# Kernel tuning notes

Hardware: AMD Instinct MI355X
Metric: run time of the kernel (lower is better)

Reference implementation:

```python
import jax, jax.numpy as jnp
import numpy as np

NUM_USERS = 100000
NUM_ITEMS = 50000
EMB = 64
N_SOC = 1000000
N_RAT = 1000000
BATCH = 16384
EPS = 1e-8


def setup_inputs() -> dict:
    key = jax.random.key(0)
    ks = jax.random.split(key, 8)
    user_emb = 0.01 * jax.random.normal(ks[0], (NUM_USERS, EMB), jnp.float32)
    item_emb = 0.01 * jax.random.normal(ks[1], (NUM_ITEMS, EMB), jnp.float32)
    users = jax.random.randint(ks[2], (BATCH,), 0, NUM_USERS)
    items = jax.random.randint(ks[3], (BATCH,), 0, NUM_ITEMS)
    social_src = jax.random.randint(ks[4], (N_SOC,), 0, NUM_USERS)
    social_dst = jax.random.randint(ks[5], (N_SOC,), 0, NUM_USERS)
    like_u = jax.random.randint(ks[6], (N_RAT,), 0, NUM_USERS)
    like_i = jax.random.randint(ks[7], (N_RAT,), 0, NUM_ITEMS)
    return {"user_emb": user_emb, "item_emb": item_emb, "users": users,
            "items": items, "social_src": social_src, "social_dst": social_dst,
            "like_u": like_u, "like_i": like_i}


def _deg(idx, num):
    # node degree as float column vector [num, 1]
    return jax.ops.segment_sum(jnp.ones((idx.shape[0],), jnp.float32), idx,
                               num_segments=num)[:, None]


def _seg_mean(msg, idx, num):
    s = jax.ops.segment_sum(msg, idx, num_segments=num)
    cnt = _deg(idx, num)
    return s / jnp.maximum(cnt, 1.0)


def reference(user_emb, item_emb, users, items, social_src, social_dst, like_u, like_i):
    # degree-based self-weights (deg=0 -> 1, deg>0 -> ~0)
    user_deg = _deg(like_u, NUM_USERS)            # out-degree on 'like'
    u_sw = 1.0 - user_deg / (user_deg + EPS)
    item_deg = _deg(like_i, NUM_ITEMS)            # out-degree on 'rev_like'
    i_sw = 1.0 - item_deg / (item_deg + EPS)

    def social_conv(hu):
        # mean aggregation over user->user social edges
        return _seg_mean(hu[social_src], social_dst, NUM_USERS)

    def rating_conv(hu, hi):
        # user <- mean of liked-item embeddings, plus degree-gated self
        new_u = u_sw * hu + _seg_mean(hi[like_i], like_u, NUM_USERS)
        new_i = i_sw * hi + _seg_mean(hu[like_u], like_i, NUM_ITEMS)
        return new_u, new_i

    # layer 1
    soc1 = social_conv(user_emb)
    rat_u1, rat_i1 = rating_conv(user_emb, item_emb)
    u1 = 0.5 * soc1 + 0.5 * rat_u1
    # layer 2 (stacked on per-branch states, as in the torch code)
    soc2 = social_conv(soc1)
    rat_u2, _ = rating_conv(rat_u1, rat_i1)
    u2 = 0.5 * soc2 + 0.5 * rat_u2

    # l_user = [0, 1, 2]
    final_user = user_emb + u1 + u2
    final_item = item_emb

    latest_user = final_user[users]
    latest_item = final_item[items]
    predict = jax.nn.sigmoid(jnp.sum(latest_user * latest_item, axis=1))
    return predict, latest_user, latest_item
```

## Files before the change

### kernel.cpp

```cpp
#include <hip/hip_runtime.h>
#include <hip/hip_bf16.h>

#define NUSERS 100000
#define NITEMS 50000
#define NEDGE  1000000
#define NBATCH 16384
#define CAP_LU 320000
#define EPB    2048
#define NBLK_E ((NEDGE + EPB - 1) / EPB)
#define NBW    3125
#define GGRID  2048
#define NB_CVT 9375
#define NB_INIT (NB_CVT + (NBATCH + 255) / 256)

#define OFF_GC     0
#define OFF_GB     768
#define OFF_GCUR   1536
#define OFF_BITS   2304
#define OFF_NEED   (OFF_BITS + 3136)
#define OFF_ZEND   (OFF_NEED + NUSERS / 4)
#define OFF_IDEG   OFF_ZEND
#define OFF_UDEG   (OFF_IDEG + NITEMS)
#define OFF_SDEG   (OFF_UDEG + NUSERS)
#define OFF_ISTART (OFF_SDEG + NUSERS)
#define OFF_USTART (OFF_ISTART + NITEMS)
#define OFF_SSTART (OFF_USTART + NUSERS)
#define OFF_UEMBH  530464
#define OFF_REC    (OFF_UEMBH + NUSERS * 32)
#define OFF_SOC1   (OFF_REC + NITEMS * 64)
#define OFF_PARTLI (OFF_SOC1 + NUSERS * 32)
#define OFF_PARTLU (OFF_PARTLI + NEDGE)
#define OFF_PARTSD (OFF_PARTLU + CAP_LU)
#define OFF_CSRLI  (OFF_PARTSD + NEDGE)
#define OFF_CSRLU  (OFF_CSRLI + NEDGE)
#define OFF_CSRSD  (OFF_CSRLU + CAP_LU)
#define WS_FLOATS  (OFF_CSRSD + NEDGE)

typedef unsigned short u16;

__device__ __forceinline__ float bf2f(u16 h) {
    union { unsigned u; float f; } c; c.u = ((unsigned)h) << 16; return c.f;
}
__device__ __forceinline__ u16 f2bf(float f) {
    union { float f; unsigned u; } c; c.f = f;
    unsigned r = c.u + 0x7fffu + ((c.u >> 16) & 1u);
    return (u16)(r >> 16);
}
__device__ __forceinline__ void acc2(unsigned w, float& a0, float& a1) {
    a0 += bf2f((u16)(w & 0xffff));
    a1 += bf2f((u16)(w >> 16));
}
__device__ __forceinline__ void acc8(uint4 w, float* a) {
    acc2(w.x, a[0], a[1]); acc2(w.y, a[2], a[3]);
    acc2(w.z, a[4], a[5]); acc2(w.w, a[6], a[7]);
}

__global__ void k_init(const float* __restrict__ uemb, const float* __restrict__ iemb,
                       const int* __restrict__ users, u16* __restrict__ uembh,
                       u16* __restrict__ rec, unsigned* __restrict__ bits,
                       unsigned char* __restrict__ needed) {
    int blk = blockIdx.x;
    if (blk < NB_CVT) {
        int t = blk * 256 + threadIdx.x;
        if (t < NUSERS * 16) {
            float4 v = ((const float4*)uemb)[t];
            ushort4 o;
            o.x = f2bf(v.x); o.y = f2bf(v.y); o.z = f2bf(v.z); o.w = f2bf(v.w);
            ((ushort4*)uembh)[t] = o;
        } else {
            int t2 = t - NUSERS * 16;
            int i = t2 >> 4, c = t2 & 15;
            float4 v = ((const float4*)iemb)[t2];
            ushort4 o;
            o.x = f2bf(v.x); o.y = f2bf(v.y); o.z = f2bf(v.z); o.w = f2bf(v.w);
            ((ushort4*)rec)[i * 32 + c] = o;
        }
    } else {
        int b = (blk - NB_CVT) * 256 + threadIdx.x;
        if (b < NBATCH) {
            int u = users[b];
            atomicOr(&bits[u >> 5], 1u << (u & 31));
            needed[u] = 1;
        }
    }
}

__global__ void k_passA(const int* __restrict__ lu, const int* __restrict__ li,
                        const int* __restrict__ sd, const int* __restrict__ ss,
                        const unsigned* __restrict__ bits, int* __restrict__ gcnt,
                        unsigned char* __restrict__ needed) {
    __shared__ int lc[768];
    __shared__ unsigned sbits[NBW];
    int t = threadIdx.x;
    for (int k = t; k < 768; k += 256) lc[k] = 0;
    for (int k = t; k < NBW; k += 256) sbits[k] = bits[k];
    __syncthreads();
    int base = blockIdx.x * EPB;
    int end = base + EPB; if (end > NEDGE) end = NEDGE;
    for (int e = base + t; e < end; e += 256) {
        int item = li[e], a = lu[e], d = sd[e];
        atomicAdd(&lc[item >> 9], 1);
        if ((sbits[a >> 5] >> (a & 31)) & 1)
            atomicAdd(&lc[256 + (a >> 9)], 1);
        atomicAdd(&lc[512 + (d >> 9)], 1);
        if ((sbits[d >> 5] >> (d & 31)) & 1)
            needed[ss[e]] = 1;
    }
    __syncthreads();
    for (int k = t; k < 768; k += 256)
        if (lc[k]) atomicAdd(&gcnt[k], lc[k]);
}

__global__ void k_passB(const int* __restrict__ gcnt, int* __restrict__ gbase,
                        int* __restrict__ gcur) {
    __shared__ int s[256];
    int t = threadIdx.x;
    for (int j = 0; j < 3; ++j) {
        int v = gcnt[j * 256 + t];
        s[t] = v;
        __syncthreads();
        for (int o = 1; o < 256; o <<= 1) {
            int x = (t >= o) ? s[t - o] : 0;
            __syncthreads();
            s[t] += x;
            __syncthreads();
        }
        int ex = s[t] - v;
        gbase[j * 256 + t] = ex;
        gcur[j * 256 + t] = ex;
        __syncthreads();
    }
}

__global__ void k_passC(const int* __restrict__ lu, const int* __restrict__ li,
                        const int* __restrict__ sd, const int* __restrict__ ss,
                        const unsigned* __restrict__ bits, int* __restrict__ gcur,
                        int* __restrict__ partLI, int* __restrict__ partLU,
                        int* __restrict__ partSD) {
    __shared__ int lc[768];
    __shared__ int go[768];
    __shared__ unsigned sbits[NBW];
    int t = threadIdx.x;
    for (int k = t; k < 768; k += 256) lc[k] = 0;
    for (int k = t; k < NBW; k += 256) sbits[k] = bits[k];
    __syncthreads();
    int base = blockIdx.x * EPB;
    int end = base + EPB; if (end > NEDGE) end = NEDGE;
    unsigned mask = 0;
    int i = 0;
    for (int e = base + t; e < end; e += 256, ++i) {
        int item = li[e], a = lu[e], d = sd[e];
        atomicAdd(&lc[item >> 9], 1);
        if ((sbits[a >> 5] >> (a & 31)) & 1) {
            atomicAdd(&lc[256 + (a >> 9)], 1);
            mask |= (1u << i);
        }
        atomicAdd(&lc[512 + (d >> 9)], 1);
    }
    __syncthreads();
    for (int k = t; k < 768; k += 256) {
        go[k] = lc[k] ? atomicAdd(&gcur[k], lc[k]) : 0;
        lc[k] = 0;
    }
    __syncthreads();
    i = 0;
    for (int e = base + t; e < end; e += 256, ++i) {
        int item = li[e], a = lu[e], d = sd[e], s_ = ss[e];
        int b0 = item >> 9;
        int r0 = atomicAdd(&lc[b0], 1);
        partLI[go[b0] + r0] = (a << 9) | (item & 511);
        if (mask & (1u << i)) {
            int b1 = 256 + (a >> 9);
            int r1 = atomicAdd(&lc[b1], 1);
            partLU[go[b1] + r1] = (item << 9) | (a & 511);
        }
        int b2 = 512 + (d >> 9);
        int r2 = atomicAdd(&lc[b2], 1);
        partSD[go[b2] + r2] = (s_ << 9) | (d & 511);
    }
}

__global__ void k_passD(const int* __restrict__ gcnt, const int* __restrict__ gbase,
                        const int* __restrict__ partLI, const int* __restrict__ partLU,
                        const int* __restrict__ partSD, int* __restrict__ csrli,
                        int* __restrict__ csrlu, int* __restrict__ csrsd,
                        int* __restrict__ ideg, int* __restrict__ udeg,
                        int* __restrict__ sdeg, int* __restrict__ istart,
                        int* __restrict__ ustart, int* __restrict__ sstart) {
    __shared__ int lcnt[512], lstart[512], sb[2][512];
    int t = threadIdx.x;
    int blk = blockIdx.x, list, b;
    const int* part; int* csr; int* deg; int* start; int n;
    if (blk < 196)      { list = 0; b = blk;       part = partLI; csr = csrli; deg = ideg; start = istart; n = NITEMS; }
    else if (blk < 392) { list = 1; b = blk - 196; part = partLU; csr = csrlu; deg = udeg; start = ustart; n = NUSERS; }
    else                { list = 2; b = blk - 392; part = partSD; csr = csrsd; deg = sdeg; start = sstart; n = NUSERS; }
    int base = gbase[list * 256 + b], cnt = gcnt[list * 256 + b];
    int node0 = b << 9;
    int M = n - node0; if (M > 512) M = 512; if (M < 0) M = 0;

    lcnt[t] = 0; lcnt[t + 256] = 0;
    __syncthreads();
    for (int i = t; i < cnt; i += 256) atomicAdd(&lcnt[part[base + i] & 511], 1);
    __syncthreads();
    sb[0][t] = lcnt[t]; sb[0][t + 256] = lcnt[t + 256];
    __syncthreads();
    int pp = 0;
    for (int o = 1; o < 512; o <<= 1) {
        int np = pp ^ 1;
        for (int k = t; k < 512; k += 256) {
            int v = sb[pp][k];
            if (k >= o) v += sb[pp][k - o];
            sb[np][k] = v;
        }
        __syncthreads();
        pp = np;
    }
    for (int k = t; k < 512; k += 256) {
        int ex = sb[pp][k] - lcnt[k];
        lstart[k] = ex;
        if (k < M) { deg[node0 + k] = lcnt[k]; start[node0 + k] = base + ex; }
    }
    __syncthreads();
    lcnt[t] = 0; lcnt[t + 256] = 0;
    __syncthreads();
    for (int i = t; i < cnt; i += 256) {
        int p = part[base + i];
        int nl = p & 511;
        int r = atomicAdd(&lcnt[nl], 1);
        csr[base + lstart[nl] + r] = p >> 9;
    }
}

__device__ __forceinline__ void item_store(int n, int dg, const float* __restrict__ iemb,
                                           u16* __restrict__ rec, int l8,
                                           const float* __restrict__ s) {
    float dgf = (float)dg;
    float inv = 1.0f / fmaxf(dgf, 1.0f);
    float sw  = 1.0f - dgf / (dgf + 1e-8f);
    float4 e0 = ((const float4*)(iemb + n * 64))[l8 * 2];
    float4 e1 = ((const float4*)(iemb + n * 64))[l8 * 2 + 1];
    uint4 o;
    o.x = (unsigned)f2bf(sw * e0.x + s[0] * inv) | ((unsigned)f2bf(sw * e0.y + s[1] * inv) << 16);
    o.y = (unsigned)f2bf(sw * e0.z + s[2] * inv) | ((unsigned)f2bf(sw * e0.w + s[3] * inv) << 16);
    o.z = (unsigned)f2bf(sw * e1.x + s[4] * inv) | ((unsigned)f2bf(sw * e1.y + s[5] * inv) << 16);
    o.w = (unsigned)f2bf(sw * e1.z + s[6] * inv) | ((unsigned)f2bf(sw * e1.w + s[7] * inv) << 16);
    ((uint4*)(rec + n * 128 + 64))[l8] = o;
}
__device__ __forceinline__ void soc_store(int n, int dg, unsigned* __restrict__ soc1, int l8,
                                          const float* __restrict__ s) {
    float inv = 1.0f / fmaxf((float)dg, 1.0f);
    uint4 o;
    o.x = (unsigned)f2bf(s[0] * inv) | ((unsigned)f2bf(s[1] * inv) << 16);
    o.y = (unsigned)f2bf(s[2] * inv) | ((unsigned)f2bf(s[3] * inv) << 16);
    o.z = (unsigned)f2bf(s[4] * inv) | ((unsigned)f2bf(s[5] * inv) << 16);
    o.w = (unsigned)f2bf(s[6] * inv) | ((unsigned)f2bf(s[7] * inv) << 16);
    ((uint4*)(soc1 + n * 32))[l8] = o;
}

__device__ __forceinline__ void gather_pair(const unsigned* __restrict__ uh32,
                                            const int* __restrict__ csr,
                                            int jA, int dA, int jB, int dB,
                                            int lane, int g, int l8,
                                            float* __restrict__ aA,
                                            float* __restrict__ aB) {
    int cA = (lane < dA) ? csr[jA + lane] : 0;
    int cB = (lane < dB) ? csr[jB + lane] : 0;
    int kmA = dA < 64 ? dA : 64;
    int kmB = dB < 64 ? dB : 64;
    int clA = kmA > 0 ? kmA - 1 : 0;
    int clB = kmB > 0 ? kmB - 1 : 0;
    int km  = kmA > kmB ? kmA : kmB;
    for (int k = 0; k < km; k += 16) {
        int q0 = k + g, q1 = k + 8 + g;
        int iA0 = q0 < kmA ? q0 : clA;
        int iA1 = q1 < kmA ? q1 : clA;
        int iB0 = q0 < kmB ? q0 : clB;
        int iB1 = q1 < kmB ? q1 : clB;
        int rA0 = __shfl(cA, iA0), rA1 = __shfl(cA, iA1);
        int rB0 = __shfl(cB, iB0), rB1 = __shfl(cB, iB1);
        uint4 wA0 = *(const uint4*)(uh32 + rA0 * 32 + l8 * 4);
        uint4 wA1 = *(const uint4*)(uh32 + rA1 * 32 + l8 * 4);
        uint4 wB0 = *(const uint4*)(uh32 + rB0 * 32 + l8 * 4);
        uint4 wB1 = *(const uint4*)(uh32 + rB1 * 32 + l8 * 4);
        if (q0 < kmA) acc8(wA0, aA);
        if (q1 < kmA) acc8(wA1, aA);
        if (q0 < kmB) acc8(wB0, aB);
        if (q1 < kmB) acc8(wB1, aB);
    }
    for (int k = 64; k < dA; k += 8) {
        int q = k + g; int idx = q < dA ? q : dA - 1;
        int r = csr[jA + idx];
        uint4 w = *(const uint4*)(uh32 + r * 32 + l8 * 4);
        if (q < dA) acc8(w, aA);
    }
    for (int k = 64; k < dB; k += 8) {
        int q = k + g; int idx = q < dB ? q : dB - 1;
        int r = csr[jB + idx];
        uint4 w = *(const uint4*)(uh32 + r * 32 + l8 * 4);
        if (q < dB) acc8(w, aB);
    }
    #pragma unroll
    for (int off = 8; off <= 32; off <<= 1) {
        #pragma unroll
        for (int m = 0; m < 8; ++m) {
            aA[m] += __shfl_xor(aA[m], off);
            aB[m] += __shfl_xor(aB[m], off);
        }
    }
}

__global__ void k_gather_fused(const float* __restrict__ iemb,
                               const unsigned* __restrict__ uh32,
                               const int* __restrict__ csrli, const int* __restrict__ istart,
                               const int* __restrict__ ideg, u16* __restrict__ rec,
                               const int* __restrict__ csrsd, const int* __restrict__ sstart,
                               const int* __restrict__ sdeg,
                               const unsigned char* __restrict__ needed,
                               unsigned* __restrict__ soc1) {
    int lane = threadIdx.x & 63;
    int wid  = blockIdx.x * 4 + (threadIdx.x >> 6);
    int nw   = gridDim.x * 4;
    int g = lane >> 3, l8 = lane & 7;
    const int NPI = NITEMS / 2;
    const int NP  = NPI + NUSERS / 2;
    for (int w = wid; w < NP; w += nw) {
        if (w < NPI) {
            int nA = w * 2, nB = nA + 1;
            int jA = istart[nA], dA = ideg[nA];
            int jB = istart[nB], dB = ideg[nB];
            float aA[8] = {0.f,0.f,0.f,0.f,0.f,0.f,0.f,0.f};
            float aB[8] = {0.f,0.f,0.f,0.f,0.f,0.f,0.f,0.f};
            gather_pair(uh32, csrli, jA, dA, jB, dB, lane, g, l8, aA, aB);
            if (g == 0)      item_store(nA, dA, iemb, rec, l8, aA);
            else if (g == 1) item_store(nB, dB, iemb, rec, l8, aB);
        } else {
            int nA = (w - NPI) * 2, nB = nA + 1;
            unsigned short nd = *(const unsigned short*)(needed + nA);
            if (!nd) continue;
            int needA = nd & 0xff, needB = nd >> 8;
            int jA = sstart[nA], dA = needA ? sdeg[nA] : 0;
            int jB = sstart[nB], dB = needB ? sdeg[nB] : 0;
            float aA[8] = {0.f,0.f,0.f,0.f,0.f,0.f,0.f,0.f};
            float aB[8] = {0.f,0.f,0.f,0.f,0.f,0.f,0.f,0.f};
            gather_pair(uh32, csrsd, jA, dA, jB, dB, lane, g, l8, aA, aB);
            if (g == 0 && needA)      soc_store(nA, dA, soc1, l8, aA);
            else if (g == 1 && needB) soc_store(nB, dB, soc1, l8, aB);
        }
    }
}

__global__ void k_final2(const int* __restrict__ users, const int* __restrict__ items,
                         const float* __restrict__ uemb, const float* __restrict__ iemb,
                         const u16* __restrict__ rec, const int* __restrict__ csrlu,
                         const int* __restrict__ ustart, const int* __restrict__ udeg,
                         const u16* __restrict__ soc1, const int* __restrict__ csrsd,
                         const int* __restrict__ sstart, const int* __restrict__ sdeg,
                         float* __restrict__ out) {
    int d   = threadIdx.x & 63;
    int wid = blockIdx.x * 4 + (threadIdx.x >> 6);
    if (wid >= NBATCH / 2) return;
    int bA = wid, bB = wid + NBATCH / 2;
    int uA = users[bA], uB = users[bB];
    int itA = items[bA], itB = items[bB];
    int juA = ustart[uA], duA = udeg[uA];
    int juB = ustart[uB], duB = udeg[uB];
    int jsA = sstart[uA], dsA = sdeg[uA];
    int jsB = sstart[uB], dsB = sdeg[uB];
    int cvUA = (d < duA) ? csrlu[juA + d] : 0;
    int cvUB = (d < duB) ? csrlu[juB + d] : 0;
    int cvSA = (d < dsA) ? csrsd[jsA + d] : 0;
    int cvSB = (d < dsB) ? csrsd[jsB + d] : 0;
    int kmuA = duA < 64 ? duA : 64, cluA = kmuA > 0 ? kmuA - 1 : 0;
    int kmuB = duB < 64 ? duB : 64, cluB = kmuB > 0 ? kmuB - 1 : 0;
    int kmu = kmuA > kmuB ? kmuA : kmuB;
    float pA0=0.f,pA1=0.f,pA2=0.f,pA3=0.f, qA0=0.f,qA1=0.f,qA2=0.f,qA3=0.f;
    float pB0=0.f,pB1=0.f,pB2=0.f,pB3=0.f, qB0=0.f,qB1=0.f,qB2=0.f,qB3=0.f;
    for (int k = 0; k < kmu; k += 4) {
        int xA0 = k   < kmuA ? k   : cluA, xA1 = k+1 < kmuA ? k+1 : cluA;
        int xA2 = k+2 < kmuA ? k+2 : cluA, xA3 = k+3 < kmuA ? k+3 : cluA;
        int xB0 = k   < kmuB ? k   : cluB, xB1 = k+1 < kmuB ? k+1 : cluB;
        int xB2 = k+2 < kmuB ? k+2 : cluB, xB3 = k+3 < kmuB ? k+3 : cluB;
        int iA0 = __shfl(cvUA, xA0), iA1 = __shfl(cvUA, xA1);
        int iA2 = __shfl(cvUA, xA2), iA3 = __shfl(cvUA, xA3);
        int iB0 = __shfl(cvUB, xB0), iB1 = __shfl(cvUB, xB1);
        int iB2 = __shfl(cvUB, xB2), iB3 = __shfl(cvUB, xB3);
        float tA0 = bf2f(rec[iA0*128 + d]),    tA1 = bf2f(rec[iA1*128 + d]);
        float tA2 = bf2f(rec[iA2*128 + d]),    tA3 = bf2f(rec[iA3*128 + d]);
        float rA0 = bf2f(rec[iA0*128 + 64 + d]), rA1 = bf2f(rec[iA1*128 + 64 + d]);
        float rA2 = bf2f(rec[iA2*128 + 64 + d]), rA3 = bf2f(rec[iA3*128 + 64 + d]);
        float tB0 = bf2f(rec[iB0*128 + d]),    tB1 = bf2f(rec[iB1*128 + d]);
        float tB2 = bf2f(rec[iB2*128 + d]),    tB3 = bf2f(rec[iB3*128 + d]);
        float rB0 = bf2f(rec[iB0*128 + 64 + d]), rB1 = bf2f(rec[iB1*128 + 64 + d]);
        float rB2 = bf2f(rec[iB2*128 + 64 + d]), rB3 = bf2f(rec[iB3*128 + 64 + d]);
        if (k   < kmuA) { pA0 += tA0; qA0 += rA0; }
        if (k+1 < kmuA) { pA1 += tA1; qA1 += rA1; }
        if (k+2 < kmuA) { pA2 += tA2; qA2 += rA2; }
        if (k+3 < kmuA) { pA3 += tA3; qA3 += rA3; }
        if (k   < kmuB) { pB0 += tB0; qB0 += rB0; }
        if (k+1 < kmuB) { pB1 += tB1; qB1 += rB1; }
        if (k+2 < kmuB) { pB2 += tB2; qB2 += rB2; }
        if (k+3 < kmuB) { pB3 += tB3; qB3 += rB3; }
    }
    for (int j = juA + 64; j < juA + duA; ++j) {
        int i0 = csrlu[j];
        pA0 += bf2f(rec[i0*128 + d]); qA0 += bf2f(rec[i0*128 + 64 + d]);
    }
    for (int j = juB + 64; j < juB + duB; ++j) {
        int i0 = csrlu[j];
        pB0 += bf2f(rec[i0*128 + d]); qB0 += bf2f(rec[i0*128 + 64 + d]);
    }
    int kmsA = dsA < 64 ? dsA : 64, clsA = kmsA > 0 ? kmsA - 1 : 0;
    int kmsB = dsB < 64 ? dsB : 64, clsB = kmsB > 0 ? kmsB - 1 : 0;
    int kms = kmsA > kmsB ? kmsA : kmsB;
    float sA0=0.f,sA1=0.f,sA2=0.f,sA3=0.f, sB0=0.f,sB1=0.f,sB2=0.f,sB3=0.f;
    for (int k = 0; k < kms; k += 4) {
        int xA0 = k   < kmsA ? k   : clsA, xA1 = k+1 < kmsA ? k+1 : clsA;
        int xA2 = k+2 < kmsA ? k+2 : clsA, xA3 = k+3 < kmsA ? k+3 : clsA;
        int xB0 = k   < kmsB ? k   : clsB, xB1 = k+1 < kmsB ? k+1 : clsB;
        int xB2 = k+2 < kmsB ? k+2 : clsB, xB3 = k+3 < kmsB ? k+3 : clsB;
        int cA0 = __shfl(cvSA, xA0), cA1 = __shfl(cvSA, xA1);
        int cA2 = __shfl(cvSA, xA2), cA3 = __shfl(cvSA, xA3);
        int cB0 = __shfl(cvSB, xB0), cB1 = __shfl(cvSB, xB1);
        int cB2 = __shfl(cvSB, xB2), cB3 = __shfl(cvSB, xB3);
        float fA0 = bf2f(soc1[cA0*64 + d]), fA1 = bf2f(soc1[cA1*64 + d]);
        float fA2 = bf2f(soc1[cA2*64 + d]), fA3 = bf2f(soc1[cA3*64 + d]);
        float fB0 = bf2f(soc1[cB0*64 + d]), fB1 = bf2f(soc1[cB1*64 + d]);
        float fB2 = bf2f(soc1[cB2*64 + d]), fB3 = bf2f(soc1[cB3*64 + d]);
        if (k   < kmsA) sA0 += fA0;
        if (k+1 < kmsA) sA1 += fA1;
        if (k+2 < kmsA) sA2 += fA2;
        if (k+3 < kmsA) sA3 += fA3;
        if (k   < kmsB) sB0 += fB0;
        if (k+1 < kmsB) sB1 += fB1;
        if (k+2 < kmsB) sB2 += fB2;
        if (k+3 < kmsB) sB3 += fB3;
    }
    for (int j = jsA + 64; j < jsA + dsA; ++j)
        sA0 += bf2f(soc1[csrsd[j]*64 + d]);
    for (int j = jsB + 64; j < jsB + dsB; ++j)
        sB0 += bf2f(soc1[csrsd[j]*64 + d]);
    {
        float invU = 1.0f / fmaxf((float)duA, 1.0f);
        float ru1 = ((pA0 + pA1) + (pA2 + pA3)) * invU;
        float ru2 = ((qA0 + qA1) + (qA2 + qA3)) * invU;
        float s2 = ((sA0 + sA1) + (sA2 + sA3)) / fmaxf((float)dsA, 1.0f);
        float ud = (float)duA;
        float usw = 1.0f - ud / (ud + 1e-8f);
        float ue = uemb[uA * 64 + d];
        float s1 = bf2f(soc1[uA * 64 + d]);
        float r1 = usw * ue + ru1;
        float r2 = usw * r1 + ru2;
        float fu = ue + 0.5f * (s1 + r1) + 0.5f * (s2 + r2);
        float iv = iemb[itA * 64 + d];
        out[NBATCH + bA * 64 + d]               = fu;
        out[NBATCH + NBATCH * 64 + bA * 64 + d] = iv;
        float p = fu * iv;
        #pragma unroll
        for (int o = 32; o > 0; o >>= 1) p += __shfl_down(p, o);
        if (d == 0) out[bA] = 1.0f / (1.0f + __expf(-p));
    }
    {
        float invU = 1.0f / fmaxf((float)duB, 1.0f);
        float ru1 = ((pB0 + pB1) + (pB2 + pB3)) * invU;
        float ru2 = ((qB0 + qB1) + (qB2 + qB3)) * invU;
        float s2 = ((sB0 + sB1) + (sB2 + sB3)) / fmaxf((float)dsB, 1.0f);
        float ud = (float)duB;
        float usw = 1.0f - ud / (ud + 1e-8f);
        float ue = uemb[uB * 64 + d];
        float s1 = bf2f(soc1[uB * 64 + d]);
        float r1 = usw * ue + ru1;
        float r2 = usw * r1 + ru2;
        float fu = ue + 0.5f * (s1 + r1) + 0.5f * (s2 + r2);
        float iv = iemb[itB * 64 + d];
        out[NBATCH + bB * 64 + d]               = fu;
        out[NBATCH + NBATCH * 64 + bB * 64 + d] = iv;
        float p = fu * iv;
        #pragma unroll
        for (int o = 32; o > 0; o >>= 1) p += __shfl_down(p, o);
        if (d == 0) out[bB] = 1.0f / (1.0f + __expf(-p));
    }
}

extern "C" void kernel_launch(void* const* d_in, const int* in_sizes, int n_in,
                              void* d_out, int out_size, void* d_ws, size_t ws_size,
                              hipStream_t stream) {
    const float* uemb  = (const float*)d_in[0];
    const float* iemb  = (const float*)d_in[1];
    const int*   users = (const int*)d_in[2];
    const int*   items = (const int*)d_in[3];
    const int*   ssrc  = (const int*)d_in[4];
    const int*   sdst  = (const int*)d_in[5];
    const int*   lu    = (const int*)d_in[6];
    const int*   li    = (const int*)d_in[7];
    float* out = (float*)d_out;

    if (ws_size < (size_t)WS_FLOATS * 4) return;

    int*           W      = (int*)d_ws;
    int*           gcnt   = W + OFF_GC;
    int*           gbase  = W + OFF_GB;
    int*           gcur   = W + OFF_GCUR;
    unsigned*      bits   = (unsigned*)(W + OFF_BITS);
    unsigned char* needed = (unsigned char*)(W + OFF_NEED);
    int*           ideg   = W + OFF_IDEG;
    int*           udeg   = W + OFF_UDEG;
    int*           sdeg   = W + OFF_SDEG;
    int*           istart = W + OFF_ISTART;
    int*           ustart = W + OFF_USTART;
    int*           sstart = W + OFF_SSTART;
    u16*           uembh  = (u16*)(W + OFF_UEMBH);
    u16*           rec    = (u16*)(W + OFF_REC);
    u16*           soc1   = (u16*)(W + OFF_SOC1);
    int*           partLI = W + OFF_PARTLI;
    int*           partLU = W + OFF_PARTLU;
    int*           partSD = W + OFF_PARTSD;
    int*           csrli  = W + OFF_CSRLI;
    int*           csrlu  = W + OFF_CSRLU;
    int*           csrsd  = W + OFF_CSRSD;

    hipMemsetAsync(d_ws, 0, (size_t)OFF_ZEND * 4, stream);

    const int B = 256;

    k_init<<<NB_INIT, B, 0, stream>>>(uemb, iemb, users, uembh, rec, bits, needed);

    k_passA<<<NBLK_E, B, 0, stream>>>(lu, li, sdst, ssrc, bits, gcnt, needed);
    k_passB<<<1, B, 0, stream>>>(gcnt, gbase, gcur);
    k_passC<<<NBLK_E, B, 0, stream>>>(lu, li, sdst, ssrc, bits, gcur,
                                      partLI, partLU, partSD);
    k_passD<<<588, B, 0, stream>>>(gcnt, gbase, partLI, partLU, partSD,
                                   csrli, csrlu, csrsd, ideg, udeg, sdeg,
                                   istart, ustart, sstart);

    k_gather_fused<<<GGRID, B, 0, stream>>>(iemb, (const unsigned*)uembh,
                                            csrli, istart, ideg, rec,
                                            csrsd, sstart, sdeg, needed,
                                            (unsigned*)soc1);

    k_final2<<<2048, B, 0, stream>>>(users, items, uemb, iemb, rec, csrlu,
                                     ustart, udeg, soc1, csrsd, sstart, sdeg, out);
}
```

Baseline: 254.2 us.

## Fuse all graph phases into one cooperative persistent kernel with grid syncs

Turns the memset plus seven separate kernel launches into a single cooperative kernel. The phases (zero/convert, slot marking, bucket count, scan, scatter, CSR build, gather, final) run as grid-stride loops separated by grid.sync(). The intent is to remove per-launch overhead and inter-kernel gaps. In exchange, parallelism is capped at the cooperative grid size (at most 1024 blocks), and the grid-wide barriers have their own cost. A non-cooperative multi-kernel fallback path is kept.

```diff
diff --git a/kernel.cpp b/kernel.cpp
--- a/kernel.cpp
+++ b/kernel.cpp
@@ -1,5 +1,8 @@
 #include <hip/hip_runtime.h>
 #include <hip/hip_bf16.h>
+#include <hip/hip_cooperative_groups.h>
+
+namespace cg = cooperative_groups;
 
 #define NUSERS 100000
 #define NITEMS 50000
@@ -10,8 +13,7 @@
 #define NBLK_E ((NEDGE + EPB - 1) / EPB)
 #define NBW    3125
 #define GGRID  2048
-#define NB_CVT 9375
-#define NB_INIT (NB_CVT + (NBATCH + 255) / 256)
+#define CGRID  1024
 
 #define OFF_GC     0
 #define OFF_GB     768
@@ -36,6 +38,8 @@
 #define OFF_CSRSD  (OFF_CSRLU + CAP_LU)
 #define WS_FLOATS  (OFF_CSRSD + NEDGE)
 
+#define SMEM_INTS  4661
+
 typedef unsigned short u16;
 
 __device__ __forceinline__ float bf2f(u16 h) {
@@ -55,13 +59,15 @@
     acc2(w.z, a[4], a[5]); acc2(w.w, a[6], a[7]);
 }
 
-__global__ void k_init(const float* __restrict__ uemb, const float* __restrict__ iemb,
-                       const int* __restrict__ users, u16* __restrict__ uembh,
-                       u16* __restrict__ rec, unsigned* __restrict__ bits,
-                       unsigned char* __restrict__ needed) {
-    int blk = blockIdx.x;
-    if (blk < NB_CVT) {
-        int t = blk * 256 + threadIdx.x;
+
+__device__ void ph_zero_cvt(const float* __restrict__ uemb, const float* __restrict__ iemb,
+                            int* __restrict__ W, u16* __restrict__ uembh,
+                            u16* __restrict__ rec) {
+    int tid = blockIdx.x * blockDim.x + threadIdx.x;
+    int nthr = gridDim.x * blockDim.x;
+    for (int k = tid; k < OFF_ZEND; k += nthr) W[k] = 0;
+    const int NT = (NUSERS + NITEMS) * 16;
+    for (int t = tid; t < NT; t += nthr) {
         if (t < NUSERS * 16) {
             float4 v = ((const float4*)uemb)[t];
             ushort4 o;
@@ -75,45 +81,53 @@
             o.x = f2bf(v.x); o.y = f2bf(v.y); o.z = f2bf(v.z); o.w = f2bf(v.w);
             ((ushort4*)rec)[i * 32 + c] = o;
         }
-    } else {
-        int b = (blk - NB_CVT) * 256 + threadIdx.x;
-        if (b < NBATCH) {
-            int u = users[b];
-            atomicOr(&bits[u >> 5], 1u << (u & 31));
-            needed[u] = 1;
-        }
-    }
-}
-
-__global__ void k_passA(const int* __restrict__ lu, const int* __restrict__ li,
-                        const int* __restrict__ sd, const int* __restrict__ ss,
-                        const unsigned* __restrict__ bits, int* __restrict__ gcnt,
+    }
+}
+
+__device__ void ph_slot(const int* __restrict__ users, unsigned* __restrict__ bits,
                         unsigned char* __restrict__ needed) {
-    __shared__ int lc[768];
-    __shared__ unsigned sbits[NBW];
+    int tid = blockIdx.x * blockDim.x + threadIdx.x;
+    int nthr = gridDim.x * blockDim.x;
+    for (int b = tid; b < NBATCH; b += nthr) {
+        int u = users[b];
+        atomicOr(&bits[u >> 5], 1u << (u & 31));
+        needed[u] = 1;
+    }
+}
+
+__device__ void ph_passA(int* __restrict__ smem, const int* __restrict__ lu,
+                         const int* __restrict__ li, const int* __restrict__ sd,
+                         const int* __restrict__ ss, const unsigned* __restrict__ bits,
+                         int* __restrict__ gcnt, unsigned char* __restrict__ needed) {
     int t = threadIdx.x;
-    for (int k = t; k < 768; k += 256) lc[k] = 0;
+    int* lc = smem;
+    unsigned* sbits = (unsigned*)(smem + 768);
     for (int k = t; k < NBW; k += 256) sbits[k] = bits[k];
-    __syncthreads();
-    int base = blockIdx.x * EPB;
-    int end = base + EPB; if (end > NEDGE) end = NEDGE;
-    for (int e = base + t; e < end; e += 256) {
-        int item = li[e], a = lu[e], d = sd[e];
-        atomicAdd(&lc[item >> 9], 1);
-        if ((sbits[a >> 5] >> (a & 31)) & 1)
-            atomicAdd(&lc[256 + (a >> 9)], 1);
-        atomicAdd(&lc[512 + (d >> 9)], 1);
-        if ((sbits[d >> 5] >> (d & 31)) & 1)
-            needed[ss[e]] = 1;
-    }
-    __syncthreads();
-    for (int k = t; k < 768; k += 256)
-        if (lc[k]) atomicAdd(&gcnt[k], lc[k]);
-}
-
-__global__ void k_passB(const int* __restrict__ gcnt, int* __restrict__ gbase,
-                        int* __restrict__ gcur) {
-    __shared__ int s[256];
+    for (int vb = blockIdx.x; vb < NBLK_E; vb += gridDim.x) {
+        for (int k = t; k < 768; k += 256) lc[k] = 0;
+        __syncthreads();
+        int base = vb * EPB;
+        int end = base + EPB; if (end > NEDGE) end = NEDGE;
+        for (int e = base + t; e < end; e += 256) {
+            int item = li[e], a = lu[e], d = sd[e];
+            atomicAdd(&lc[item >> 9], 1);
+            if ((sbits[a >> 5] >> (a & 31)) & 1)
+                atomicAdd(&lc[256 + (a >> 9)], 1);
+            atomicAdd(&lc[512 + (d >> 9)], 1);
+            if ((sbits[d >> 5] >> (d & 31)) & 1)
+                needed[ss[e]] = 1;
+        }
+        __syncthreads();
+        for (int k = t; k < 768; k += 256)
+            if (lc[k]) atomicAdd(&gcnt[k], lc[k]);
+        __syncthreads();
+    }
+}
+
+__device__ void ph_passB(const int* __restrict__ gcnt, int* __restrict__ gbase,
+                         int* __restrict__ gcur, int* __restrict__ smem) {
+    if (blockIdx.x != 0) return;
+    int* s = smem;
     int t = threadIdx.x;
     for (int j = 0; j < 3; ++j) {
         int v = gcnt[j * 256 + t];
@@ -132,102 +146,110 @@
     }
 }
 
-__global__ void k_passC(const int* __restrict__ lu, const int* __restrict__ li,
-                        const int* __restrict__ sd, const int* __restrict__ ss,
-                        const unsigned* __restrict__ bits, int* __restrict__ gcur,
-                        int* __restrict__ partLI, int* __restrict__ partLU,
-                        int* __restrict__ partSD) {
-    __shared__ int lc[768];
-    __shared__ int go[768];
-    __shared__ unsigned sbits[NBW];
+__device__ void ph_passC(int* __restrict__ smem, const int* __restrict__ lu,
+                         const int* __restrict__ li, const int* __restrict__ sd,
+                         const int* __restrict__ ss, const unsigned* __restrict__ bits,
+                         int* __restrict__ gcur, int* __restrict__ partLI,
+                         int* __restrict__ partLU, int* __restrict__ partSD) {
     int t = threadIdx.x;
-    for (int k = t; k < 768; k += 256) lc[k] = 0;
+    int* lc = smem;
+    int* go = smem + 768;
+    unsigned* sbits = (unsigned*)(smem + 1536);
     for (int k = t; k < NBW; k += 256) sbits[k] = bits[k];
-    __syncthreads();
-    int base = blockIdx.x * EPB;
-    int end = base + EPB; if (end > NEDGE) end = NEDGE;
-    unsigned mask = 0;
-    int i = 0;
-    for (int e = base + t; e < end; e += 256, ++i) {
-        int item = li[e], a = lu[e], d = sd[e];
-        atomicAdd(&lc[item >> 9], 1);
-        if ((sbits[a >> 5] >> (a & 31)) & 1) {
-            atomicAdd(&lc[256 + (a >> 9)], 1);
-            mask |= (1u << i);
-        }
-        atomicAdd(&lc[512 + (d >> 9)], 1);
-    }
-    __syncthreads();
-    for (int k = t; k < 768; k += 256) {
-        go[k] = lc[k] ? atomicAdd(&gcur[k], lc[k]) : 0;
-        lc[k] = 0;
-    }
-    __syncthreads();
-    i = 0;
-    for (int e = base + t; e < end; e += 256, ++i) {
-        int item = li[e], a = lu[e], d = sd[e], s_ = ss[e];
-        int b0 = item >> 9;
-        int r0 = atomicAdd(&lc[b0], 1);
-        partLI[go[b0] + r0] = (a << 9) | (item & 511);
-        if (mask & (1u << i)) {
-            int b1 = 256 + (a >> 9);
-            int r1 = atomicAdd(&lc[b1], 1);
-            partLU[go[b1] + r1] = (item << 9) | (a & 511);
-        }
-        int b2 = 512 + (d >> 9);
-        int r2 = atomicAdd(&lc[b2], 1);
-        partSD[go[b2] + r2] = (s_ << 9) | (d & 511);
-    }
-}
-
-__global__ void k_passD(const int* __restrict__ gcnt, const int* __restrict__ gbase,
-                        const int* __restrict__ partLI, const int* __restrict__ partLU,
-                        const int* __restrict__ partSD, int* __restrict__ csrli,
-                        int* __restrict__ csrlu, int* __restrict__ csrsd,
-                        int* __restrict__ ideg, int* __restrict__ udeg,
-                        int* __restrict__ sdeg, int* __restrict__ istart,
-                        int* __restrict__ ustart, int* __restrict__ sstart) {
-    __shared__ int lcnt[512], lstart[512], sb[2][512];
+    for (int vb = blockIdx.x; vb < NBLK_E; vb += gridDim.x) {
+        for (int k = t; k < 768; k += 256) lc[k] = 0;
+        __syncthreads();
+        int base = vb * EPB;
+        int end = base + EPB; if (end > NEDGE) end = NEDGE;
+        unsigned mask = 0;
+        int i = 0;
+        for (int e = base + t; e < end; e += 256, ++i) {
+            int item = li[e], a = lu[e], d = sd[e];
+            atomicAdd(&lc[item >> 9], 1);
+            if ((sbits[a >> 5] >> (a & 31)) & 1) {
+                atomicAdd(&lc[256 + (a >> 9)], 1);
+                mask |= (1u << i);
+            }
+            atomicAdd(&lc[512 + (d >> 9)], 1);
+        }
+        __syncthreads();
+        for (int k = t; k < 768; k += 256) {
+            go[k] = lc[k] ? atomicAdd(&gcur[k], lc[k]) : 0;
+            lc[k] = 0;
+        }
+        __syncthreads();
+        i = 0;
+        for (int e = base + t; e < end; e += 256, ++i) {
+            int item = li[e], a = lu[e], d = sd[e], s_ = ss[e];
+            int b0 = item >> 9;
+            int r0 = atomicAdd(&lc[b0], 1);
+            partLI[go[b0] + r0] = (a << 9) | (item & 511);
+            if (mask & (1u << i)) {
+                int b1 = 256 + (a >> 9);
+                int r1 = atomicAdd(&lc[b1], 1);
+                partLU[go[b1] + r1] = (item << 9) | (a & 511);
+            }
+            int b2 = 512 + (d >> 9);
+            int r2 = atomicAdd(&lc[b2], 1);
+            partSD[go[b2] + r2] = (s_ << 9) | (d & 511);
+        }
+        __syncthreads();
+    }
+}
+
+__device__ void ph_passD(int* __restrict__ smem, const int* __restrict__ gcnt,
+                         const int* __restrict__ gbase, const int* __restrict__ partLI,
+                         const int* __restrict__ partLU, const int* __restrict__ partSD,
+                         int* __restrict__ csrli, int* __restrict__ csrlu,
+                         int* __restrict__ csrsd, int* __restrict__ ideg,
+                         int* __restrict__ udeg, int* __restrict__ sdeg,
+                         int* __restrict__ istart, int* __restrict__ ustart,
+                         int* __restrict__ sstart) {
     int t = threadIdx.x;
-    int blk = blockIdx.x, list, b;
-    const int* part; int* csr; int* deg; int* start; int n;
-    if (blk < 196)      { list = 0; b = blk;       part = partLI; csr = csrli; deg = ideg; start = istart; n = NITEMS; }
-    else if (blk < 392) { list = 1; b = blk - 196; part = partLU; csr = csrlu; deg = udeg; start = ustart; n = NUSERS; }
-    else                { list = 2; b = blk - 392; part = partSD; csr = csrsd; deg = sdeg; start = sstart; n = NUSERS; }
-    int base = gbase[list * 256 + b], cnt = gcnt[list * 256 + b];
-    int node0 = b << 9;
-    int M = n - node0; if (M > 512) M = 512; if (M < 0) M = 0;
-
-    lcnt[t] = 0; lcnt[t + 256] = 0;
-    __syncthreads();
-    for (int i = t; i < cnt; i += 256) atomicAdd(&lcnt[part[base + i] & 511], 1);
-    __syncthreads();
-    sb[0][t] = lcnt[t]; sb[0][t + 256] = lcnt[t + 256];
-    __syncthreads();
-    int pp = 0;
-    for (int o = 1; o < 512; o <<= 1) {
-        int np = pp ^ 1;
+    int* lcnt = smem;
+    int* lstart = smem + 512;
+    for (int blk = blockIdx.x; blk < 588; blk += gridDim.x) {
+        int list, b;
+        const int* part; int* csr; int* deg; int* start; int n;
+        if (blk < 196)      { list = 0; b = blk;       part = partLI; csr = csrli; deg = ideg; start = istart; n = NITEMS; }
+        else if (blk < 392) { list = 1; b = blk - 196; part = partLU; csr = csrlu; deg = udeg; start = ustart; n = NUSERS; }
+        else                { list = 2; b = blk - 392; part = partSD; csr = csrsd; deg = sdeg; start = sstart; n = NUSERS; }
+        int base = gbase[list * 256 + b], cnt = gcnt[list * 256 + b];
+        int node0 = b << 9;
+        int M = n - node0; if (M > 512) M = 512; if (M < 0) M = 0;
+
+        lcnt[t] = 0; lcnt[t + 256] = 0;
+        __syncthreads();
+        for (int i = t; i < cnt; i += 256) atomicAdd(&lcnt[part[base + i] & 511], 1);
+        __syncthreads();
+        int* ps = smem + 1024;
+        int* pd = smem + 1536;
+        ps[t] = lcnt[t]; ps[t + 256] = lcnt[t + 256];
+        __syncthreads();
+        for (int o = 1; o < 512; o <<= 1) {
+            for (int k = t; k < 512; k += 256) {
+                int v = ps[k];
+                if (k >= o) v += ps[k - o];
+                pd[k] = v;
+            }
+            __syncthreads();
+            int* tmp = ps; ps = pd; pd = tmp;
+        }
         for (int k = t; k < 512; k += 256) {
-            int v = sb[pp][k];
-            if (k >= o) v += sb[pp][k - o];
-            sb[np][k] = v;
-        }
-        __syncthreads();
-        pp = np;
-    }
-    for (int k = t; k < 512; k += 256) {
-        int ex = sb[pp][k] - lcnt[k];
-        lstart[k] = ex;
-        if (k < M) { deg[node0 + k] = lcnt[k]; start[node0 + k] = base + ex; }
-    }
-    __syncthreads();
-    lcnt[t] = 0; lcnt[t + 256] = 0;
-    __syncthreads();
-    for (int i = t; i < cnt; i += 256) {
-        int p = part[base + i];
-        int nl = p & 511;
-        int r = atomicAdd(&lcnt[nl], 1);
-        csr[base + lstart[nl] + r] = p >> 9;
+            int ex = ps[k] - lcnt[k];
+            lstart[k] = ex;
+            if (k < M) { deg[node0 + k] = lcnt[k]; start[node0 + k] = base + ex; }
+        }
+        __syncthreads();
+        lcnt[t] = 0; lcnt[t + 256] = 0;
+        __syncthreads();
+        for (int i = t; i < cnt; i += 256) {
+            int p = part[base + i];
+            int nl = p & 511;
+            int r = atomicAdd(&lcnt[nl], 1);
+            csr[base + lstart[nl] + r] = p >> 9;
+        }
+        __syncthreads();
     }
 }
 
@@ -309,14 +331,13 @@
     }
 }
 
-__global__ void k_gather_fused(const float* __restrict__ iemb,
-                               const unsigned* __restrict__ uh32,
-                               const int* __restrict__ csrli, const int* __restrict__ istart,
-                               const int* __restrict__ ideg, u16* __restrict__ rec,
-                               const int* __restrict__ csrsd, const int* __restrict__ sstart,
-                               const int* __restrict__ sdeg,
-                               const unsigned char* __restrict__ needed,
-                               unsigned* __restrict__ soc1) {
+__device__ void ph_gather(const float* __restrict__ iemb, const unsigned* __restrict__ uh32,
+                          const int* __restrict__ csrli, const int* __restrict__ istart,
+                          const int* __restrict__ ideg, u16* __restrict__ rec,
+                          const int* __restrict__ csrsd, const int* __restrict__ sstart,
+                          const int* __restrict__ sdeg,
+                          const unsigned char* __restrict__ needed,
+                          unsigned* __restrict__ soc1) {
     int lane = threadIdx.x & 63;
     int wid  = blockIdx.x * 4 + (threadIdx.x >> 6);
     int nw   = gridDim.x * 4;
@@ -349,154 +370,147 @@
     }
 }
 
-__global__ void k_final2(const int* __restrict__ users, const int* __restrict__ items,
+__device__ void ph_final(const int* __restrict__ users, const int* __restrict__ items,
                          const float* __restrict__ uemb, const float* __restrict__ iemb,
                          const u16* __restrict__ rec, const int* __restrict__ csrlu,
                          const int* __restrict__ ustart, const int* __restrict__ udeg,
                          const u16* __restrict__ soc1, const int* __restrict__ csrsd,
                          const int* __restrict__ sstart, const int* __restrict__ sdeg,
                          float* __restrict__ out) {
-    int d   = threadIdx.x & 63;
-    int wid = blockIdx.x * 4 + (threadIdx.x >> 6);
-    if (wid >= NBATCH / 2) return;
-    int bA = wid, bB = wid + NBATCH / 2;
-    int uA = users[bA], uB = users[bB];
-    int itA = items[bA], itB = items[bB];
-    int juA = ustart[uA], duA = udeg[uA];
-    int juB = ustart[uB], duB = udeg[uB];
-    int jsA = sstart[uA], dsA = sdeg[uA];
-    int jsB = sstart[uB], dsB = sdeg[uB];
-    int cvUA = (d < duA) ? csrlu[juA + d] : 0;
-    int cvUB = (d < duB) ? csrlu[juB + d] : 0;
-    int cvSA = (d < dsA) ? csrsd[jsA + d] : 0;
-    int cvSB = (d < dsB) ? csrsd[jsB + d] : 0;
-    int kmuA = duA < 64 ? duA : 64, cluA = kmuA > 0 ? kmuA - 1 : 0;
-    int kmuB = duB < 64 ? duB : 64, cluB = kmuB > 0 ? kmuB - 1 : 0;
-    int kmu = kmuA > kmuB ? kmuA : kmuB;
-    float pA0=0.f,pA1=0.f,pA2=0.f,pA3=0.f, qA0=0.f,qA1=0.f,qA2=0.f,qA3=0.f;
-    float pB0=0.f,pB1=0.f,pB2=0.f,pB3=0.f, qB0=0.f,qB1=0.f,qB2=0.f,qB3=0.f;
-    for (int k = 0; k < kmu; k += 4) {
-        int xA0 = k   < kmuA ? k   : cluA, xA1 = k+1 < kmuA ? k+1 : cluA;
-        int xA2 = k+2 < kmuA ? k+2 : cluA, xA3 = k+3 < kmuA ? k+3 : cluA;
-        int xB0 = k   < kmuB ? k   : cluB, xB1 = k+1 < kmuB ? k+1 : cluB;
-        int xB2 = k+2 < kmuB ? k+2 : cluB, xB3 = k+3 < kmuB ? k+3 : cluB;
-        int iA0 = __shfl(cvUA, xA0), iA1 = __shfl(cvUA, xA1);
-        int iA2 = __shfl(cvUA, xA2), iA3 = __shfl(cvUA, xA3);
-        int iB0 = __shfl(cvUB, xB0), iB1 = __shfl(cvUB, xB1);
-        int iB2 = __shfl(cvUB, xB2), iB3 = __shfl(cvUB, xB3);
-        float tA0 = bf2f(rec[iA0*128 + d]),    tA1 = bf2f(rec[iA1*128 + d]);
-        float tA2 = bf2f(rec[iA2*128 + d]),    tA3 = bf2f(rec[iA3*128 + d]);
-        float rA0 = bf2f(rec[iA0*128 + 64 + d]), rA1 = bf2f(rec[iA1*128 + 64 + d]);
-        float rA2 = bf2f(rec[iA2*128 + 64 + d]), rA3 = bf2f(rec[iA3*128 + 64 + d]);
-        float tB0 = bf2f(rec[iB0*128 + d]),    tB1 = bf2f(rec[iB1*128 + d]);
-        float tB2 = bf2f(rec[iB2*128 + d]),    tB3 = bf2f(rec[iB3*128 + d]);
-        float rB0 = bf2f(rec[iB0*128 + 64 + d]), rB1 = bf2f(rec[iB1*128 + 64 + d]);
-        float rB2 = bf2f(rec[iB2*128 + 64 + d]), rB3 = bf2f(rec[iB3*128 + 64 + d]);
-        if (k   < kmuA) { pA0 += tA0; qA0 += rA0; }
-        if (k+1 < kmuA) { pA1 += tA1; qA1 += rA1; }
-        if (k+2 < kmuA) { pA2 += tA2; qA2 += rA2; }
-        if (k+3 < kmuA) { pA3 += tA3; qA3 += rA3; }
-        if (k   < kmuB) { pB0 += tB0; qB0 += rB0; }
-        if (k+1 < kmuB) { pB1 += tB1; qB1 += rB1; }
-        if (k+2 < kmuB) { pB2 += tB2; qB2 += rB2; }
-        if (k+3 < kmuB) { pB3 += tB3; qB3 += rB3; }
-    }
-    for (int j = juA + 64; j < juA + duA; ++j) {
-        int i0 = csrlu[j];
-        pA0 += bf2f(rec[i0*128 + d]); qA0 += bf2f(rec[i0*128 + 64 + d]);
-    }
-    for (int j = juB + 64; j < juB + duB; ++j) {
-        int i0 = csrlu[j];
-        pB0 += bf2f(rec[i0*128 + d]); qB0 += bf2f(rec[i0*128 + 64 + d]);
-    }
-    int kmsA = dsA < 64 ? dsA : 64, clsA = kmsA > 0 ? kmsA - 1 : 0;
-    int kmsB = dsB < 64 ? dsB : 64, clsB = kmsB > 0 ? kmsB - 1 : 0;
-    int kms = kmsA > kmsB ? kmsA : kmsB;
-    float sA0=0.f,sA1=0.f,sA2=0.f,sA3=0.f, sB0=0.f,sB1=0.f,sB2=0.f,sB3=0.f;
-    for (int k = 0; k < kms; k += 4) {
-        int xA0 = k   < kmsA ? k   : clsA, xA1 = k+1 < kmsA ? k+1 : clsA;
-        int xA2 = k+2 < kmsA ? k+2 : clsA, xA3 = k+3 < kmsA ? k+3 : clsA;
-        int xB0 = k   < kmsB ? k   : clsB, xB1 = k+1 < kmsB ? k+1 : clsB;
-        int xB2 = k+2 < kmsB ? k+2 : clsB, xB3 = k+3 < kmsB ? k+3 : clsB;
-        int cA0 = __shfl(cvSA, xA0), cA1 = __shfl(cvSA, xA1);
-        int cA2 = __shfl(cvSA, xA2), cA3 = __shfl(cvSA, xA3);
-        int cB0 = __shfl(cvSB, xB0), cB1 = __shfl(cvSB, xB1);
-        int cB2 = __shfl(cvSB, xB2), cB3 = __shfl(cvSB, xB3);
-        float fA0 = bf2f(soc1[cA0*64 + d]), fA1 = bf2f(soc1[cA1*64 + d]);
-        float fA2 = bf2f(soc1[cA2*64 + d]), fA3 = bf2f(soc1[cA3*64 + d]);
-        float fB0 = bf2f(soc1[cB0*64 + d]), fB1 = bf2f(soc1[cB1*64 + d]);
-        float fB2 = bf2f(soc1[cB2*64 + d]), fB3 = bf2f(soc1[cB3*64 + d]);
-        if (k   < kmsA) sA0 += fA0;
-        if (k+1 < kmsA) sA1 += fA1;
-        if (k+2 < kmsA) sA2 += fA2;
-        if (k+3 < kmsA) sA3 += fA3;
-        if (k   < kmsB) sB0 += fB0;
-        if (k+1 < kmsB) sB1 += fB1;
-        if (k+2 < kmsB) sB2 += fB2;
-        if (k+3 < kmsB) sB3 += fB3;
-    }
-    for (int j = jsA + 64; j < jsA + dsA; ++j)
-        sA0 += bf2f(soc1[csrsd[j]*64 + d]);
-    for (int j = jsB + 64; j < jsB + dsB; ++j)
-        sB0 += bf2f(soc1[csrsd[j]*64 + d]);
-    {
-        float invU = 1.0f / fmaxf((float)duA, 1.0f);
-        float ru1 = ((pA0 + pA1) + (pA2 + pA3)) * invU;
-        float ru2 = ((qA0 + qA1) + (qA2 + qA3)) * invU;
-        float s2 = ((sA0 + sA1) + (sA2 + sA3)) / fmaxf((float)dsA, 1.0f);
-        float ud = (float)duA;
-        float usw = 1.0f - ud / (ud + 1e-8f);
-        float ue = uemb[uA * 64 + d];
-        float s1 = bf2f(soc1[uA * 64 + d]);
-        float r1 = usw * ue + ru1;
-        float r2 = usw * r1 + ru2;
-        float fu = ue + 0.5f * (s1 + r1) + 0.5f * (s2 + r2);
-        float iv = iemb[itA * 64 + d];
-        out[NBATCH + bA * 64 + d]               = fu;
-        out[NBATCH + NBATCH * 64 + bA * 64 + d] = iv;
-        float p = fu * iv;
-        #pragma unroll
-        for (int o = 32; o > 0; o >>= 1) p += __shfl_down(p, o);
-        if (d == 0) out[bA] = 1.0f / (1.0f + __expf(-p));
-    }
-    {
-        float invU = 1.0f / fmaxf((float)duB, 1.0f);
-        float ru1 = ((pB0 + pB1) + (pB2 + pB3)) * invU;
-        float ru2 = ((qB0 + qB1) + (qB2 + qB3)) * invU;
-        float s2 = ((sB0 + sB1) + (sB2 + sB3)) / fmaxf((float)dsB, 1.0f);
-        float ud = (float)duB;
-        float usw = 1.0f - ud / (ud + 1e-8f);
-        float ue = uemb[uB * 64 + d];
-        float s1 = bf2f(soc1[uB * 64 + d]);
-        float r1 = usw * ue + ru1;
-        float r2 = usw * r1 + ru2;
-        float fu = ue + 0.5f * (s1 + r1) + 0.5f * (s2 + r2);
-        float iv = iemb[itB * 64 + d];
-        out[NBATCH + bB * 64 + d]               = fu;
-        out[NBATCH + NBATCH * 64 + bB * 64 + d] = iv;
-        float p = fu * iv;
-        #pragma unroll
-        for (int o = 32; o > 0; o >>= 1) p += __shfl_down(p, o);
-        if (d == 0) out[bB] = 1.0f / (1.0f + __expf(-p));
-    }
-}
-
-extern "C" void kernel_launch(void* const* d_in, const int* in_sizes, int n_in,
-                              void* d_out, int out_size, void* d_ws, size_t ws_size,
-                              hipStream_t stream) {
-    const float* uemb  = (const float*)d_in[0];
-    const float* iemb  = (const float*)d_in[1];
-    const int*   users = (const int*)d_in[2];
-    const int*   items = (const int*)d_in[3];
-    const int*   ssrc  = (const int*)d_in[4];
-    const int*   sdst  = (const int*)d_in[5];
-    const int*   lu    = (const int*)d_in[6];
-    const int*   li    = (const int*)d_in[7];
-    float* out = (float*)d_out;
-
-    if (ws_size < (size_t)WS_FLOATS * 4) return;
-
-    int*           W      = (int*)d_ws;
+    int d    = threadIdx.x & 63;
+    int wid0 = blockIdx.x * 4 + (threadIdx.x >> 6);
+    int nw   = gridDim.x * 4;
+    for (int wid = wid0; wid < NBATCH / 2; wid += nw) {
+        int bA = wid, bB = wid + NBATCH / 2;
+        int uA = users[bA], uB = users[bB];
+        int itA = items[bA], itB = items[bB];
+        int juA = ustart[uA], duA = udeg[uA];
+        int juB = ustart[uB], duB = udeg[uB];
+        int jsA = sstart[uA], dsA = sdeg[uA];
+        int jsB = sstart[uB], dsB = sdeg[uB];
+        int cvUA = (d < duA) ? csrlu[juA + d] : 0;
+        int cvUB = (d < duB) ? csrlu[juB + d] : 0;
+        int cvSA = (d < dsA) ? csrsd[jsA + d] : 0;
+        int cvSB = (d < dsB) ? csrsd[jsB + d] : 0;
+        int kmuA = duA < 64 ? duA : 64, cluA = kmuA > 0 ? kmuA - 1 : 0;
+        int kmuB = duB < 64 ? duB : 64, cluB = kmuB > 0 ? kmuB - 1 : 0;
+        int kmu = kmuA > kmuB ? kmuA : kmuB;
+        float pA0=0.f,pA1=0.f,pA2=0.f,pA3=0.f, qA0=0.f,qA1=0.f,qA2=0.f,qA3=0.f;
+        float pB0=0.f,pB1=0.f,pB2=0.f,pB3=0.f, qB0=0.f,qB1=0.f,qB2=0.f,qB3=0.f;
+        for (int k = 0; k < kmu; k += 4) {
+            int xA0 = k   < kmuA ? k   : cluA, xA1 = k+1 < kmuA ? k+1 : cluA;
+            int xA2 = k+2 < kmuA ? k+2 : cluA, xA3 = k+3 < kmuA ? k+3 : cluA;
+            int xB0 = k   < kmuB ? k   : cluB, xB1 = k+1 < kmuB ? k+1 : cluB;
+            int xB2 = k+2 < kmuB ? k+2 : cluB, xB3 = k+3 < kmuB ? k+3 : cluB;
+            int iA0 = __shfl(cvUA, xA0), iA1 = __shfl(cvUA, xA1);
+            int iA2 = __shfl(cvUA, xA2), iA3 = __shfl(cvUA, xA3);
+            int iB0 = __shfl(cvUB, xB0), iB1 = __shfl(cvUB, xB1);
+            int iB2 = __shfl(cvUB, xB2), iB3 = __shfl(cvUB, xB3);
+            float tA0 = bf2f(rec[iA0*128 + d]),      tA1 = bf2f(rec[iA1*128 + d]);
+            float tA2 = bf2f(rec[iA2*128 + d]),      tA3 = bf2f(rec[iA3*128 + d]);
+            float rA0 = bf2f(rec[iA0*128 + 64 + d]), rA1 = bf2f(rec[iA1*128 + 64 + d]);
+            float rA2 = bf2f(rec[iA2*128 + 64 + d]), rA3 = bf2f(rec[iA3*128 + 64 + d]);
+            float tB0 = bf2f(rec[iB0*128 + d]),      tB1 = bf2f(rec[iB1*128 + d]);
+            float tB2 = bf2f(rec[iB2*128 + d]),      tB3 = bf2f(rec[iB3*128 + d]);
+            float rB0 = bf2f(rec[iB0*128 + 64 + d]), rB1 = bf2f(rec[iB1*128 + 64 + d]);
+            float rB2 = bf2f(rec[iB2*128 + 64 + d]), rB3 = bf2f(rec[iB3*128 + 64 + d]);
+            if (k   < kmuA) { pA0 += tA0; qA0 += rA0; }
+            if (k+1 < kmuA) { pA1 += tA1; qA1 += rA1; }
+            if (k+2 < kmuA) { pA2 += tA2; qA2 += rA2; }
+            if (k+3 < kmuA) { pA3 += tA3; qA3 += rA3; }
+            if (k   < kmuB) { pB0 += tB0; qB0 += rB0; }
+            if (k+1 < kmuB) { pB1 += tB1; qB1 += rB1; }
+            if (k+2 < kmuB) { pB2 += tB2; qB2 += rB2; }
+            if (k+3 < kmuB) { pB3 += tB3; qB3 += rB3; }
+        }
+        for (int j = juA + 64; j < juA + duA; ++j) {
+            int i0 = csrlu[j];
+            pA0 += bf2f(rec[i0*128 + d]); qA0 += bf2f(rec[i0*128 + 64 + d]);
+        }
+        for (int j = juB + 64; j < juB + duB; ++j) {
+            int i0 = csrlu[j];
+            pB0 += bf2f(rec[i0*128 + d]); qB0 += bf2f(rec[i0*128 + 64 + d]);
+        }
+        int kmsA = dsA < 64 ? dsA : 64, clsA = kmsA > 0 ? kmsA - 1 : 0;
+        int kmsB = dsB < 64 ? dsB : 64, clsB = kmsB > 0 ? kmsB - 1 : 0;
+        int kms = kmsA > kmsB ? kmsA : kmsB;
+        float sA0=0.f,sA1=0.f,sA2=0.f,sA3=0.f, sB0=0.f,sB1=0.f,sB2=0.f,sB3=0.f;
+        for (int k = 0; k < kms; k += 4) {
+            int xA0 = k   < kmsA ? k   : clsA, xA1 = k+1 < kmsA ? k+1 : clsA;
+            int xA2 = k+2 < kmsA ? k+2 : clsA, xA3 = k+3 < kmsA ? k+3 : clsA;
+            int xB0 = k   < kmsB ? k   : clsB, xB1 = k+1 < kmsB ? k+1 : clsB;
+            int xB2 = k+2 < kmsB ? k+2 : clsB, xB3 = k+3 < kmsB ? k+3 : clsB;
+            int cA0 = __shfl(cvSA, xA0), cA1 = __shfl(cvSA, xA1);
+            int cA2 = __shfl(cvSA, xA2), cA3 = __shfl(cvSA, xA3);
+            int cB0 = __shfl(cvSB, xB0), cB1 = __shfl(cvSB, xB1);
+            int cB2 = __shfl(cvSB, xB2), cB3 = __shfl(cvSB, xB3);
+            float fA0 = bf2f(soc1[cA0*64 + d]), fA1 = bf2f(soc1[cA1*64 + d]);
+            float fA2 = bf2f(soc1[cA2*64 + d]), fA3 = bf2f(soc1[cA3*64 + d]);
+            float fB0 = bf2f(soc1[cB0*64 + d]), fB1 = bf2f(soc1[cB1*64 + d]);
+            float fB2 = bf2f(soc1[cB2*64 + d]), fB3 = bf2f(soc1[cB3*64 + d]);
+            if (k   < kmsA) sA0 += fA0;
+            if (k+1 < kmsA) sA1 += fA1;
+            if (k+2 < kmsA) sA2 += fA2;
+            if (k+3 < kmsA) sA3 += fA3;
+            if (k   < kmsB) sB0 += fB0;
+            if (k+1 < kmsB) sB1 += fB1;
+            if (k+2 < kmsB) sB2 += fB2;
+            if (k+3 < kmsB) sB3 += fB3;
+        }
+        for (int j = jsA + 64; j < jsA + dsA; ++j)
+            sA0 += bf2f(soc1[csrsd[j]*64 + d]);
+        for (int j = jsB + 64; j < jsB + dsB; ++j)
+            sB0 += bf2f(soc1[csrsd[j]*64 + d]);
+        {
+            float invU = 1.0f / fmaxf((float)duA, 1.0f);
+            float ru1 = ((pA0 + pA1) + (pA2 + pA3)) * invU;
+            float ru2 = ((qA0 + qA1) + (qA2 + qA3)) * invU;
+            float s2 = ((sA0 + sA1) + (sA2 + sA3)) / fmaxf((float)dsA, 1.0f);
+            float ud = (float)duA;
+            float usw = 1.0f - ud / (ud + 1e-8f);
+            float ue = uemb[uA * 64 + d];
+            float s1 = bf2f(soc1[uA * 64 + d]);
+            float r1 = usw * ue + ru1;
+            float r2 = usw * r1 + ru2;
+            float fu = ue + 0.5f * (s1 + r1) + 0.5f * (s2 + r2);
+            float iv = iemb[itA * 64 + d];
+            out[NBATCH + bA * 64 + d]               = fu;
+            out[NBATCH + NBATCH * 64 + bA * 64 + d] = iv;
+            float p = fu * iv;
+            #pragma unroll
+            for (int o = 32; o > 0; o >>= 1) p += __shfl_down(p, o);
+            if (d == 0) out[bA] = 1.0f / (1.0f + __expf(-p));
+        }
+        {
+            float invU = 1.0f / fmaxf((float)duB, 1.0f);
+            float ru1 = ((pB0 + pB1) + (pB2 + pB3)) * invU;
+            float ru2 = ((qB0 + qB1) + (qB2 + qB3)) * invU;
+            float s2 = ((sB0 + sB1) + (sB2 + sB3)) / fmaxf((float)dsB, 1.0f);
+            float ud = (float)duB;
+            float usw = 1.0f - ud / (ud + 1e-8f);
+            float ue = uemb[uB * 64 + d];
+            float s1 = bf2f(soc1[uB * 64 + d]);
+            float r1 = usw * ue + ru1;
+            float r2 = usw * r1 + ru2;
+            float fu = ue + 0.5f * (s1 + r1) + 0.5f * (s2 + r2);
+            float iv = iemb[itB * 64 + d];
+            out[NBATCH + bB * 64 + d]               = fu;
+            out[NBATCH + NBATCH * 64 + bB * 64 + d] = iv;
+            float p = fu * iv;
+            #pragma unroll
+            for (int o = 32; o > 0; o >>= 1) p += __shfl_down(p, o);
+            if (d == 0) out[bB] = 1.0f / (1.0f + __expf(-p));
+        }
+    }
+}
+
+__global__ void __launch_bounds__(256, 4)
+k_mega(const float* uemb, const float* iemb, const int* users, const int* items,
+       const int* ssrc, const int* sdst, const int* lu, const int* li,
+       int* W, float* out) {
+    __shared__ int smem[SMEM_INTS];
+    cg::grid_group grid = cg::this_grid();
+
     int*           gcnt   = W + OFF_GC;
     int*           gbase  = W + OFF_GB;
     int*           gcur   = W + OFF_GCUR;
@@ -518,25 +532,123 @@
     int*           csrlu  = W + OFF_CSRLU;
     int*           csrsd  = W + OFF_CSRSD;
 
-    hipMemsetAsync(d_ws, 0, (size_t)OFF_ZEND * 4, stream);
+    ph_zero_cvt(uemb, iemb, W, uembh, rec);
+    grid.sync();
+    ph_slot(users, bits, needed);
+    grid.sync();
+    ph_passA(smem, lu, li, sdst, ssrc, bits, gcnt, needed);
+    grid.sync();
+    ph_passB(gcnt, gbase, gcur, smem);
+    grid.sync();
+    ph_passC(smem, lu, li, sdst, ssrc, bits, gcur, partLI, partLU, partSD);
+    grid.sync();
+    ph_passD(smem, gcnt, gbase, partLI, partLU, partSD, csrli, csrlu, csrsd,
+             ideg, udeg, sdeg, istart, ustart, sstart);
+    grid.sync();
+    ph_gather(iemb, (const unsigned*)uembh, csrli, istart, ideg, rec,
+              csrsd, sstart, sdeg, needed, soc1 ? (unsigned*)soc1 : nullptr);
+    grid.sync();
+    ph_final(users, items, uemb, iemb, rec, csrlu, ustart, udeg,
+             soc1, csrsd, sstart, sdeg, out);
+}
+
+__global__ void __launch_bounds__(256) k_f_zero(const float* uemb, const float* iemb, int* W) {
+    ph_zero_cvt(uemb, iemb, W, (u16*)(W + OFF_UEMBH), (u16*)(W + OFF_REC));
+}
+__global__ void __launch_bounds__(256) k_f_slot(const int* users, int* W) {
+    ph_slot(users, (unsigned*)(W + OFF_BITS), (unsigned char*)(W + OFF_NEED));
+}
+__global__ void __launch_bounds__(256) k_f_passA(const int* lu, const int* li,
+                                                 const int* sd, const int* ss, int* W) {
+    __shared__ int smem[SMEM_INTS];
+    ph_passA(smem, lu, li, sd, ss, (unsigned*)(W + OFF_BITS), W + OFF_GC,
+             (unsigned char*)(W + OFF_NEED));
+}
+__global__ void __launch_bounds__(256) k_f_passB(int* W) {
+    __shared__ int smem[256];
+    ph_passB(W + OFF_GC, W + OFF_GB, W + OFF_GCUR, smem);
+}
+__global__ void __launch_bounds__(256) k_f_passC(const int* lu, const int* li,
+                                                 const int* sd, const int* ss, int* W) {
+    __shared__ int smem[SMEM_INTS];
+    ph_passC(smem, lu, li, sd, ss, (unsigned*)(W + OFF_BITS), W + OFF_GCUR,
+             W + OFF_PARTLI, W + OFF_PARTLU, W + OFF_PARTSD);
+}
+__global__ void __launch_bounds__(256) k_f_passD(int* W) {
+    __shared__ int smem[SMEM_INTS];
+    ph_passD(smem, W + OFF_GC, W + OFF_GB, W + OFF_PARTLI, W + OFF_PARTLU,
+             W + OFF_PARTSD, W + OFF_CSRLI, W + OFF_CSRLU, W + OFF_CSRSD,
+             W + OFF_IDEG, W + OFF_UDEG, W + OFF_SDEG,
+             W + OFF_ISTART, W + OFF_USTART, W + OFF_SSTART);
+}
+__global__ void __launch_bounds__(256) k_f_gather(const float* iemb, int* W) {
+    ph_gather(iemb, (const unsigned*)(W + OFF_UEMBH), W + OFF_CSRLI, W + OFF_ISTART,
+              W + OFF_IDEG, (u16*)(W + OFF_REC), W + OFF_CSRSD, W + OFF_SSTART,
+              W + OFF_SDEG, (unsigned char*)(W + OFF_NEED), (unsigned*)(W + OFF_SOC1));
+}
+__global__ void __launch_bounds__(256) k_f_final(const int* users, const int* items,
+                                                 const float* uemb, const float* iemb,
+                                                 int* W, float* out) {
+    ph_final(users, items, uemb, iemb, (const u16*)(W + OFF_REC), W + OFF_CSRLU,
+             W + OFF_USTART, W + OFF_UDEG, (const u16*)(W + OFF_SOC1), W + OFF_CSRSD,
+             W + OFF_SSTART, W + OFF_SDEG, out);
+}
+
+extern "C" void kernel_launch(void* const* d_in, const int* in_sizes, int n_in,
+                              void* d_out, int out_size, void* d_ws, size_t ws_size,
+                              hipStream_t stream) {
+    const float* uemb  = (const float*)d_in[0];
+    const float* iemb  = (const float*)d_in[1];
+    const int*   users = (const int*)d_in[2];
+    const int*   items = (const int*)d_in[3];
+    const int*   ssrc  = (const int*)d_in[4];
+    const int*   sdst  = (const int*)d_in[5];
+    const int*   lu    = (const int*)d_in[6];
+    const int*   li    = (const int*)d_in[7];
+    float* out = (float*)d_out;
+
+    if (ws_size < (size_t)WS_FLOATS * 4) return;
+
+    int* W = (int*)d_ws;
+
+    static int coop_grid = -2;
+    if (coop_grid == -2) {
+        int dev = 0;
+        hipDeviceProp_t prop;
+        int nb = 0;
+        if (hipGetDevice(&dev) == hipSuccess &&
+            hipGetDeviceProperties(&prop, dev) == hipSuccess &&
+            prop.cooperativeLaunch &&
+            hipOccupancyMaxActiveBlocksPerMultiprocessor(&nb, k_mega, 256, 0) == hipSuccess &&
+            nb > 0) {
+            long g = (long)nb * prop.multiProcessorCount;
+            coop_grid = (int)(g < CGRID ? g : CGRID);
+        } else {
+            coop_grid = -1;
+        }
+        (void)hipGetLastError();
+    }
+
+    if (coop_grid > 0) {
+        const float* a0 = uemb; const float* a1 = iemb;
+        const int* a2 = users; const int* a3 = items;
+        const int* a4 = ssrc;  const int* a5 = sdst;
+        const int* a6 = lu;    const int* a7 = li;
+        int* a8 = W; float* a9 = out;
+        void* args[] = { &a0, &a1, &a2, &a3, &a4, &a5, &a6, &a7, &a8, &a9 };
+        hipError_t e = hipLaunchCooperativeKernel(k_mega, dim3(coop_grid), dim3(256),
+                                                  args, 0, stream);
+        if (e == hipSuccess) return;
+        (void)hipGetLastError();
+    }
 
     const int B = 256;
-
-    k_init<<<NB_INIT, B, 0, stream>>>(uemb, iemb, users, uembh, rec, bits, needed);
-
-    k_passA<<<NBLK_E, B, 0, stream>>>(lu, li, sdst, ssrc, bits, gcnt, needed);
-    k_passB<<<1, B, 0, stream>>>(gcnt, gbase, gcur);
-    k_passC<<<NBLK_E, B, 0, stream>>>(lu, li, sdst, ssrc, bits, gcur,
-                                      partLI, partLU, partSD);
-    k_passD<<<588, B, 0, stream>>>(gcnt, gbase, partLI, partLU, partSD,
-                                   csrli, csrlu, csrsd, ideg, udeg, sdeg,
-                                   istart, ustart, sstart);
-
-    k_gather_fused<<<GGRID, B, 0, stream>>>(iemb, (const unsigned*)uembh,
-                                            csrli, istart, ideg, rec,
-                                            csrsd, sstart, sdeg, needed,
-                                            (unsigned*)soc1);
-
-    k_final2<<<2048, B, 0, stream>>>(users, items, uemb, iemb, rec, csrlu,
-                                     ustart, udeg, soc1, csrsd, sstart, sdeg, out);
-}
+    k_f_zero<<<2048, B, 0, stream>>>(uemb, iemb, W);
+    k_f_slot<<<64, B, 0, stream>>>(users, W);
+    k_f_passA<<<NBLK_E, B, 0, stream>>>(lu, li, sdst, ssrc, W);
+    k_f_passB<<<1, B, 0, stream>>>(W);
+    k_f_passC<<<NBLK_E, B, 0, stream>>>(lu, li, sdst, ssrc, W);
+    k_f_passD<<<588, B, 0, stream>>>(W);
+    k_f_gather<<<GGRID, B, 0, stream>>>(iemb, W);
+    k_f_final<<<GGRID, B, 0, stream>>>(users, items, uemb, iemb, W, out);
+}
```

New measurement: 724.2 us. 185% more time.
